# Kernel optimization log

Measured on AMD Instinct MI355X. Metric: run time of the kernel, lower is better.

## Reference

```python
import jax, jax.numpy as jnp
import numpy as np

N = 100000      # nodes
E = 3200000     # edges (avg degree 32)
NFEAT = 512
HID = 64
NCLASS = 64
ALPHA = 0.1
NITER = 10


def setup_inputs() -> dict:
    key = jax.random.key(0)
    k1, k2, k3, k4, k5 = jax.random.split(key, 5)
    x = jax.random.normal(k1, (N, NFEAT), dtype=jnp.float32)
    edge_index = jax.random.randint(k2, (2, E), 0, N, dtype=jnp.int32)
    edge_weight = jax.random.uniform(k3, (E,), dtype=jnp.float32)
    W1 = jax.random.normal(k4, (NFEAT, HID), dtype=jnp.float32) * 0.05
    W2 = jax.random.normal(k5, (HID, NCLASS), dtype=jnp.float32) * 0.05
    return {"x": x, "edge_index": edge_index, "edge_weight": edge_weight,
            "W1": W1, "W2": W2}


def reference(x, edge_index, edge_weight, W1, W2):
    # _transform_features (eval mode: dropout = identity, bias=False)
    h = jax.nn.relu(x @ W1)            # [N, HID]
    z0 = h @ W2                        # [N, NCLASS]
    src = edge_index[0]
    dst = edge_index[1]
    z = z0
    # APPNP power iteration: z = adj @ z + alpha * z0
    for _ in range(NITER):
        msg = edge_weight[:, None] * z[src]                          # [E, NCLASS]
        z = jax.ops.segment_sum(msg, dst, num_segments=N) + ALPHA * z0
    return jax.nn.log_softmax(z, axis=-1)
```

## Files before the change

kernel.cpp:

```cpp
#include <hip/hip_runtime.h>

#define NN     100000
#define EE     3200000
#define NF     512
#define HIDN   64
#define NCLS   64
#define ALPHA  0.1f

#define CHUNK  512
#define NB     196

#define SC_BLOCKS 2048

typedef unsigned short ushort_t;
typedef unsigned int   uint_t;

__device__ inline ushort_t f2bf(float f)
{
    uint_t u = __float_as_uint(f);
    u += 0x7FFFu + ((u >> 16) & 1u);
    return (ushort_t)(u >> 16);
}
__device__ inline float bf2f(ushort_t b)
{
    return __uint_as_float(((uint_t)b) << 16);
}

__device__ inline int2 ldnt_e(const int2* p)
{
    unsigned long long v =
        __builtin_nontemporal_load((const unsigned long long*)p);
    int2 r;
    r.x = (int)(v & 0xFFFFFFFFull);
    r.y = (int)(v >> 32);
    return r;
}

template <bool RELU>
__global__ __launch_bounds__(256) void gemm_kernel(
    const float* __restrict__ A, const float* __restrict__ B,
    float* __restrict__ C, int nrows, int K)
{
    const int BK = 16;
    __shared__ float AsT[BK][68];
    __shared__ float Bs [BK][68];

    int tid = threadIdx.x;
    int tx  = tid & 15;
    int ty  = tid >> 4;
    int rowBase = blockIdx.x * 64;

    int arow = tid >> 2;
    int ak   = (tid & 3) * 4;
    int brow = tid >> 4;
    int bcol = (tid & 15) * 4;

    float acc[4][4] = {};

    for (int k0 = 0; k0 < K; k0 += BK) {
        float4 av;
        int gr = rowBase + arow;
        if (gr < nrows) av = *(const float4*)(A + (size_t)gr * K + k0 + ak);
        else            av = make_float4(0.f, 0.f, 0.f, 0.f);
        float4 bv = *(const float4*)(B + (size_t)(k0 + brow) * 64 + bcol);

        __syncthreads();
        AsT[ak + 0][arow] = av.x;
        AsT[ak + 1][arow] = av.y;
        AsT[ak + 2][arow] = av.z;
        AsT[ak + 3][arow] = av.w;
        *(float4*)&Bs[brow][bcol] = bv;
        __syncthreads();

#pragma unroll
        for (int kk = 0; kk < BK; ++kk) {
            float4 a = *(const float4*)&AsT[kk][ty * 4];
            float4 b = *(const float4*)&Bs [kk][tx * 4];
            acc[0][0] = fmaf(a.x, b.x, acc[0][0]);
            acc[0][1] = fmaf(a.x, b.y, acc[0][1]);
            acc[0][2] = fmaf(a.x, b.z, acc[0][2]);
            acc[0][3] = fmaf(a.x, b.w, acc[0][3]);
            acc[1][0] = fmaf(a.y, b.x, acc[1][0]);
            acc[1][1] = fmaf(a.y, b.y, acc[1][1]);
            acc[1][2] = fmaf(a.y, b.z, acc[1][2]);
            acc[1][3] = fmaf(a.y, b.w, acc[1][3]);
            acc[2][0] = fmaf(a.z, b.x, acc[2][0]);
            acc[2][1] = fmaf(a.z, b.y, acc[2][1]);
            acc[2][2] = fmaf(a.z, b.z, acc[2][2]);
            acc[2][3] = fmaf(a.z, b.w, acc[2][3]);
            acc[3][0] = fmaf(a.w, b.x, acc[3][0]);
            acc[3][1] = fmaf(a.w, b.y, acc[3][1]);
            acc[3][2] = fmaf(a.w, b.z, acc[3][2]);
            acc[3][3] = fmaf(a.w, b.w, acc[3][3]);
        }
    }

#pragma unroll
    for (int i = 0; i < 4; ++i) {
        int r = rowBase + ty * 4 + i;
        if (r < nrows) {
            float4 o;
            o.x = acc[i][0]; o.y = acc[i][1]; o.z = acc[i][2]; o.w = acc[i][3];
            if (RELU) {
                o.x = fmaxf(o.x, 0.f); o.y = fmaxf(o.y, 0.f);
                o.z = fmaxf(o.z, 0.f); o.w = fmaxf(o.w, 0.f);
            }
            *(float4*)(C + (size_t)r * 64 + tx * 4) = o;
        }
    }
}

__global__ __launch_bounds__(256) void gemm2_kernel(
    const float* __restrict__ A, const float* __restrict__ B,
    ushort_t* __restrict__ zb, ushort_t* __restrict__ az, int nrows, int K)
{
    const int BK = 16;
    __shared__ float AsT[BK][68];
    __shared__ float Bs [BK][68];

    int tid = threadIdx.x;
    int tx  = tid & 15;
    int ty  = tid >> 4;
    int rowBase = blockIdx.x * 64;

    int arow = tid >> 2;
    int ak   = (tid & 3) * 4;
    int brow = tid >> 4;
    int bcol = (tid & 15) * 4;

    float acc[4][4] = {};

    for (int k0 = 0; k0 < K; k0 += BK) {
        float4 av;
        int gr = rowBase + arow;
        if (gr < nrows) av = *(const float4*)(A + (size_t)gr * K + k0 + ak);
        else            av = make_float4(0.f, 0.f, 0.f, 0.f);
        float4 bv = *(const float4*)(B + (size_t)(k0 + brow) * 64 + bcol);

        __syncthreads();
        AsT[ak + 0][arow] = av.x;
        AsT[ak + 1][arow] = av.y;
        AsT[ak + 2][arow] = av.z;
        AsT[ak + 3][arow] = av.w;
        *(float4*)&Bs[brow][bcol] = bv;
        __syncthreads();

#pragma unroll
        for (int kk = 0; kk < BK; ++kk) {
            float4 a = *(const float4*)&AsT[kk][ty * 4];
            float4 b = *(const float4*)&Bs [kk][tx * 4];
            acc[0][0] = fmaf(a.x, b.x, acc[0][0]);
            acc[0][1] = fmaf(a.x, b.y, acc[0][1]);
            acc[0][2] = fmaf(a.x, b.z, acc[0][2]);
            acc[0][3] = fmaf(a.x, b.w, acc[0][3]);
            acc[1][0] = fmaf(a.y, b.x, acc[1][0]);
            acc[1][1] = fmaf(a.y, b.y, acc[1][1]);
            acc[1][2] = fmaf(a.y, b.z, acc[1][2]);
            acc[1][3] = fmaf(a.y, b.w, acc[1][3]);
            acc[2][0] = fmaf(a.z, b.x, acc[2][0]);
            acc[2][1] = fmaf(a.z, b.y, acc[2][1]);
            acc[2][2] = fmaf(a.z, b.z, acc[2][2]);
            acc[2][3] = fmaf(a.z, b.w, acc[2][3]);
            acc[3][0] = fmaf(a.w, b.x, acc[3][0]);
            acc[3][1] = fmaf(a.w, b.y, acc[3][1]);
            acc[3][2] = fmaf(a.w, b.z, acc[3][2]);
            acc[3][3] = fmaf(a.w, b.w, acc[3][3]);
        }
    }

#pragma unroll
    for (int i = 0; i < 4; ++i) {
        int r = rowBase + ty * 4 + i;
        if (r < nrows) {
            ushort4 o, oa;
            o.x  = f2bf(acc[i][0]);         o.y  = f2bf(acc[i][1]);
            o.z  = f2bf(acc[i][2]);         o.w  = f2bf(acc[i][3]);
            oa.x = f2bf(ALPHA * acc[i][0]); oa.y = f2bf(ALPHA * acc[i][1]);
            oa.z = f2bf(ALPHA * acc[i][2]); oa.w = f2bf(ALPHA * acc[i][3]);
            *(ushort4*)(zb + (size_t)r * 64 + tx * 4) = o;
            *(ushort4*)(az + (size_t)r * 64 + tx * 4) = oa;
        }
    }
}

__global__ __launch_bounds__(256) void zero_kernel(int* __restrict__ p, int n)
{
    int i = blockIdx.x * 256 + threadIdx.x;
    if (i < n) p[i] = 0;
}

__global__ __launch_bounds__(256) void count_kernel(const int* __restrict__ dst,
                                                    int* __restrict__ deg)
{
    int e = blockIdx.x * 256 + threadIdx.x;
    if (e < EE) atomicAdd(&deg[dst[e]], 1);
}

__global__ __launch_bounds__(256) void scanA_kernel(const int* __restrict__ deg,
                                                    int* __restrict__ bsum)
{
    int b = blockIdx.x, t = threadIdx.x;
    int i = b * CHUNK + t * 2;
    int v = 0;
    if (i < NN)     v += deg[i];
    if (i + 1 < NN) v += deg[i + 1];
    __shared__ int sm[256];
    sm[t] = v;
    __syncthreads();
    for (int o = 128; o > 0; o >>= 1) {
        if (t < o) sm[t] += sm[t + o];
        __syncthreads();
    }
    if (t == 0) bsum[b] = sm[0];
}

__global__ __launch_bounds__(256) void scanB_kernel(const int* __restrict__ bsum,
                                                    int* __restrict__ bbase,
                                                    int* __restrict__ offs)
{
    int t = threadIdx.x;
    int v = (t < NB) ? bsum[t] : 0;
    __shared__ int sm[256];
    sm[t] = v;
    __syncthreads();
    for (int o = 1; o < 256; o <<= 1) {
        int u = (t >= o) ? sm[t - o] : 0;
        __syncthreads();
        sm[t] += u;
        __syncthreads();
    }
    if (t < NB) bbase[t] = sm[t] - v;
    if (t == 0) offs[NN] = EE;
}

__global__ __launch_bounds__(256) void scanC_kernel(const int* __restrict__ deg,
                                                    const int* __restrict__ bbase,
                                                    int* __restrict__ offs,
                                                    int* __restrict__ cursor)
{
    int b = blockIdx.x, t = threadIdx.x;
    int i0 = b * CHUNK + t * 2;
    int d0 = (i0 < NN)     ? deg[i0]     : 0;
    int d1 = (i0 + 1 < NN) ? deg[i0 + 1] : 0;
    int local = d0 + d1;
    __shared__ int sm[256];
    sm[t] = local;
    __syncthreads();
    for (int o = 1; o < 256; o <<= 1) {
        int u = (t >= o) ? sm[t - o] : 0;
        __syncthreads();
        sm[t] += u;
        __syncthreads();
    }
    int excl = sm[t] - local + bbase[b];
    if (i0 < NN)     { offs[i0]     = excl;      cursor[i0]     = excl;      }
    if (i0 + 1 < NN) { offs[i0 + 1] = excl + d0; cursor[i0 + 1] = excl + d0; }
}

__global__ __launch_bounds__(256) void scatter_kernel(
    const int* __restrict__ src, const int* __restrict__ dst,
    const float* __restrict__ w, int* cursor, int2* __restrict__ csr)
{
    const int x      = blockIdx.x & 7;
    const int lo     = x * (NN / 8);
    const int hi     = lo + (NN / 8);
    const int nsl    = gridDim.x >> 3;
    const int stride = nsl * 256;
    for (int e = (blockIdx.x >> 3) * 256 + threadIdx.x; e < EE; e += stride) {
        int d = dst[e];
        if (d >= lo && d < hi) {
            int pos = atomicAdd(&cursor[d], 1);
            csr[pos] = make_int2(src[e], __float_as_int(w[e]));
        }
    }
}

template <bool LSM>
__global__ __launch_bounds__(256) void propagate_kernel(
    const ushort_t* __restrict__ zin, const ushort_t* __restrict__ az0,
    ushort_t* __restrict__ zout_b, float* __restrict__ zout_f,
    const int* __restrict__ offs, const int2* __restrict__ csr)
{
    int gid  = blockIdx.x * 256 + threadIdx.x;
    int node = gid >> 6;
    int lane = gid & 63;
    if (node >= NN) return;

    int beg = offs[node];
    int end = offs[node + 1];
    float acc = 0.f;
    int j = beg;
    for (; j + 8 <= end; j += 8) {
        int2 e0 = ldnt_e(csr + j);     int2 e1 = ldnt_e(csr + j + 1);
        int2 e2 = ldnt_e(csr + j + 2); int2 e3 = ldnt_e(csr + j + 3);
        int2 e4 = ldnt_e(csr + j + 4); int2 e5 = ldnt_e(csr + j + 5);
        int2 e6 = ldnt_e(csr + j + 6); int2 e7 = ldnt_e(csr + j + 7);
        float v0 = bf2f(zin[(size_t)e0.x * 64 + lane]);
        float v1 = bf2f(zin[(size_t)e1.x * 64 + lane]);
        float v2 = bf2f(zin[(size_t)e2.x * 64 + lane]);
        float v3 = bf2f(zin[(size_t)e3.x * 64 + lane]);
        float v4 = bf2f(zin[(size_t)e4.x * 64 + lane]);
        float v5 = bf2f(zin[(size_t)e5.x * 64 + lane]);
        float v6 = bf2f(zin[(size_t)e6.x * 64 + lane]);
        float v7 = bf2f(zin[(size_t)e7.x * 64 + lane]);
        acc = fmaf(__int_as_float(e0.y), v0, acc);
        acc = fmaf(__int_as_float(e1.y), v1, acc);
        acc = fmaf(__int_as_float(e2.y), v2, acc);
        acc = fmaf(__int_as_float(e3.y), v3, acc);
        acc = fmaf(__int_as_float(e4.y), v4, acc);
        acc = fmaf(__int_as_float(e5.y), v5, acc);
        acc = fmaf(__int_as_float(e6.y), v6, acc);
        acc = fmaf(__int_as_float(e7.y), v7, acc);
    }
    for (; j < end; ++j) {
        int2 e = ldnt_e(csr + j);
        acc = fmaf(__int_as_float(e.y), bf2f(zin[(size_t)e.x * 64 + lane]), acc);
    }

    float out = acc + bf2f(az0[(size_t)node * 64 + lane]);

    if (LSM) {
        float m = out;
#pragma unroll
        for (int o = 32; o > 0; o >>= 1) m = fmaxf(m, __shfl_xor(m, o, 64));
        float e = __expf(out - m);
        float s = e;
#pragma unroll
        for (int o = 32; o > 0; o >>= 1) s += __shfl_xor(s, o, 64);
        __builtin_nontemporal_store((out - m) - __logf(s),
                                    zout_f + (size_t)node * 64 + lane);
    } else {
        __builtin_nontemporal_store(f2bf(out),
                                    zout_b + (size_t)node * 64 + lane);
    }
}

extern "C" void kernel_launch(void* const* d_in, const int* in_sizes, int n_in,
                              void* d_out, int out_size, void* d_ws, size_t ws_size,
                              hipStream_t stream)
{
    const float* x  = (const float*)d_in[0];
    const int*   ei = (const int*)  d_in[1];
    const float* ew = (const float*)d_in[2];
    const float* W1 = (const float*)d_in[3];
    const float* W2 = (const float*)d_in[4];
    const int* src = ei;
    const int* dst = ei + EE;

    char* ws = (char*)d_ws;
    size_t off = 0;
    auto alloc = [&](size_t bytes) -> char* {
        char* p = ws + off;
        off += (bytes + 255) & ~(size_t)255;
        return p;
    };

    float*    h     = (float*)   alloc((size_t)NN * HIDN * 4);
    ushort_t* zbA   = (ushort_t*)alloc((size_t)NN * NCLS * 2);
    ushort_t* zbB   = (ushort_t*)alloc((size_t)NN * NCLS * 2);
    ushort_t* az0   = (ushort_t*)alloc((size_t)NN * NCLS * 2);
    int*      deg   = (int*)     alloc((size_t)NN * 4);
    int*      offs  = (int*)     alloc((size_t)(NN + 1) * 4);
    int*      cur_  = (int*)     alloc((size_t)NN * 4);
    int*      bsum  = (int*)     alloc((size_t)NB * 4);
    int*      bbase = (int*)     alloc((size_t)NB * 4);

    int2* csr = (int2*)h;

    gemm_kernel<true><<<(NN + 63) / 64, 256, 0, stream>>>(x, W1, h, NN, NF);
    gemm2_kernel<<<(NN + 63) / 64, 256, 0, stream>>>(h, W2, zbA, az0, NN, HIDN);

    zero_kernel<<<(NN + 255) / 256, 256, 0, stream>>>(deg, NN);
    count_kernel<<<EE / 256, 256, 0, stream>>>(dst, deg);
    scanA_kernel<<<NB, 256, 0, stream>>>(deg, bsum);
    scanB_kernel<<<1, 256, 0, stream>>>(bsum, bbase, offs);
    scanC_kernel<<<NB, 256, 0, stream>>>(deg, bbase, offs, cur_);
    scatter_kernel<<<SC_BLOCKS, 256, 0, stream>>>(src, dst, ew, cur_, csr);

    const ushort_t* cur = zbA;
    ushort_t* nxt = zbB;
    for (int it = 0; it < 9; ++it) {
        propagate_kernel<false><<<(NN * 64) / 256, 256, 0, stream>>>(
            cur, az0, nxt, nullptr, offs, csr);
        ushort_t* t = (ushort_t*)cur; cur = nxt; nxt = t;
    }
    propagate_kernel<true><<<(NN * 64) / 256, 256, 0, stream>>>(
        cur, az0, nullptr, (float*)d_out, offs, csr);
}
```

Measured before the change: 1.885 ms.

## Split node features into 16-class column slabs assigned per XCD for L2 locality

Stores z and alpha*z0 as four column chunks of 16 classes each, and maps blocks so that each pair of XCDs handles one chunk. The gather working set per XCD then shrinks to about 3.2MB and can stay in that XCD's L2. Each wave processes one node with four edge slots in parallel and reduces them with shuffles. Log-softmax moves to a separate kernel because a node's classes are now spread across different blocks. This adds an extra f32 buffer and an extra launch, and each gathered row read is only 32 bytes.

```diff
diff --git a/kernel.cpp b/kernel.cpp
--- a/kernel.cpp
+++ b/kernel.cpp
@@ -7,6 +7,9 @@
 #define NCLS   64
 #define ALPHA  0.1f
 
+#define NC     4
+#define CW     16
+
 #define CHUNK  512
 #define NB     196
 
@@ -34,6 +37,10 @@
     r.x = (int)(v & 0xFFFFFFFFull);
     r.y = (int)(v >> 32);
     return r;
+}
+__device__ inline ushort_t ldnt_u16(const ushort_t* p)
+{
+    return __builtin_nontemporal_load(p);
 }
 
 template <bool RELU>
@@ -168,6 +175,8 @@
         }
     }
 
+    int c = tx >> 2;
+    int k = (tx & 3) * 4;
 #pragma unroll
     for (int i = 0; i < 4; ++i) {
         int r = rowBase + ty * 4 + i;
@@ -177,8 +186,9 @@
             o.z  = f2bf(acc[i][2]);         o.w  = f2bf(acc[i][3]);
             oa.x = f2bf(ALPHA * acc[i][0]); oa.y = f2bf(ALPHA * acc[i][1]);
             oa.z = f2bf(ALPHA * acc[i][2]); oa.w = f2bf(ALPHA * acc[i][3]);
-            *(ushort4*)(zb + (size_t)r * 64 + tx * 4) = o;
-            *(ushort4*)(az + (size_t)r * 64 + tx * 4) = oa;
+            size_t o16 = (size_t)c * (NN * CW) + (size_t)r * CW + k;
+            *(ushort4*)(zb + o16) = o;
+            *(ushort4*)(az + o16) = oa;
         }
     }
 }
@@ -275,64 +285,80 @@
     }
 }
 
-template <bool LSM>
+template <bool FINAL>
 __global__ __launch_bounds__(256) void propagate_kernel(
-    const ushort_t* __restrict__ zin, const ushort_t* __restrict__ az0,
-    ushort_t* __restrict__ zout_b, float* __restrict__ zout_f,
+    const ushort_t* __restrict__ zin,
+    const ushort_t* __restrict__ az0,
+    ushort_t* __restrict__ zout,
+    float* __restrict__ zf,
     const int* __restrict__ offs, const int2* __restrict__ csr)
 {
-    int gid  = blockIdx.x * 256 + threadIdx.x;
-    int node = gid >> 6;
-    int lane = gid & 63;
-    if (node >= NN) return;
+    int bid   = blockIdx.x;
+    int xcd   = bid & 7;
+    int c     = xcd >> 1;
+    int half  = xcd & 1;
+    int g     = bid >> 3;
+    int wave  = threadIdx.x >> 6;
+    int lane  = threadIdx.x & 63;
+    int node  = ((g * 2 + half) << 2) + wave;
+    int cls   = lane & 15;
+    int eslot = lane >> 4;
+
+    const ushort_t* zt = zin + (size_t)c * (NN * CW);
 
     int beg = offs[node];
     int end = offs[node + 1];
     float acc = 0.f;
     int j = beg;
     for (; j + 8 <= end; j += 8) {
-        int2 e0 = ldnt_e(csr + j);     int2 e1 = ldnt_e(csr + j + 1);
-        int2 e2 = ldnt_e(csr + j + 2); int2 e3 = ldnt_e(csr + j + 3);
-        int2 e4 = ldnt_e(csr + j + 4); int2 e5 = ldnt_e(csr + j + 5);
-        int2 e6 = ldnt_e(csr + j + 6); int2 e7 = ldnt_e(csr + j + 7);
-        float v0 = bf2f(zin[(size_t)e0.x * 64 + lane]);
-        float v1 = bf2f(zin[(size_t)e1.x * 64 + lane]);
-        float v2 = bf2f(zin[(size_t)e2.x * 64 + lane]);
-        float v3 = bf2f(zin[(size_t)e3.x * 64 + lane]);
-        float v4 = bf2f(zin[(size_t)e4.x * 64 + lane]);
-        float v5 = bf2f(zin[(size_t)e5.x * 64 + lane]);
-        float v6 = bf2f(zin[(size_t)e6.x * 64 + lane]);
-        float v7 = bf2f(zin[(size_t)e7.x * 64 + lane]);
+        int2 e0 = ldnt_e(csr + j + eslot);
+        int2 e1 = ldnt_e(csr + j + 4 + eslot);
+        float v0 = bf2f(zt[(size_t)e0.x * CW + cls]);
+        float v1 = bf2f(zt[(size_t)e1.x * CW + cls]);
         acc = fmaf(__int_as_float(e0.y), v0, acc);
         acc = fmaf(__int_as_float(e1.y), v1, acc);
-        acc = fmaf(__int_as_float(e2.y), v2, acc);
-        acc = fmaf(__int_as_float(e3.y), v3, acc);
-        acc = fmaf(__int_as_float(e4.y), v4, acc);
-        acc = fmaf(__int_as_float(e5.y), v5, acc);
-        acc = fmaf(__int_as_float(e6.y), v6, acc);
-        acc = fmaf(__int_as_float(e7.y), v7, acc);
-    }
-    for (; j < end; ++j) {
-        int2 e = ldnt_e(csr + j);
-        acc = fmaf(__int_as_float(e.y), bf2f(zin[(size_t)e.x * 64 + lane]), acc);
-    }
-
-    float out = acc + bf2f(az0[(size_t)node * 64 + lane]);
-
-    if (LSM) {
-        float m = out;
-#pragma unroll
-        for (int o = 32; o > 0; o >>= 1) m = fmaxf(m, __shfl_xor(m, o, 64));
-        float e = __expf(out - m);
-        float s = e;
-#pragma unroll
-        for (int o = 32; o > 0; o >>= 1) s += __shfl_xor(s, o, 64);
-        __builtin_nontemporal_store((out - m) - __logf(s),
-                                    zout_f + (size_t)node * 64 + lane);
-    } else {
-        __builtin_nontemporal_store(f2bf(out),
-                                    zout_b + (size_t)node * 64 + lane);
-    }
+    }
+    if (j + 4 <= end) {
+        int2 e = ldnt_e(csr + j + eslot);
+        acc = fmaf(__int_as_float(e.y), bf2f(zt[(size_t)e.x * CW + cls]), acc);
+        j += 4;
+    }
+    int r = end - j;
+    if (eslot < r) {
+        int2 e = ldnt_e(csr + j + eslot);
+        acc = fmaf(__int_as_float(e.y), bf2f(zt[(size_t)e.x * CW + cls]), acc);
+    }
+    acc += __shfl_xor(acc, 16, 64);
+    acc += __shfl_xor(acc, 32, 64);
+
+    size_t o16 = (size_t)c * (NN * CW) + (size_t)node * CW + cls;
+    float out = acc + bf2f(ldnt_u16(az0 + o16));
+    if (eslot == 0) {
+        if (FINAL) zf[o16] = out;
+        else       __builtin_nontemporal_store(f2bf(out), zout + o16);
+    }
+}
+
+template <typename T>
+__global__ __launch_bounds__(256) void lsm_kernel(
+    const T* __restrict__ zf, float* __restrict__ out)
+{
+    int gid  = blockIdx.x * 256 + threadIdx.x;
+    int node = gid >> 6;
+    int lane = gid & 63;
+    if (node >= NN) return;
+    size_t o16 = (size_t)(lane >> 4) * (NN * CW) + (size_t)node * CW + (lane & 15);
+    float v;
+    if (sizeof(T) == 2) v = bf2f(*(const ushort_t*)(zf + o16));
+    else                v = *(const float*)(zf + o16);
+    float m = v;
+#pragma unroll
+    for (int o = 32; o > 0; o >>= 1) m = fmaxf(m, __shfl_xor(m, o, 64));
+    float e = __expf(v - m);
+    float s = e;
+#pragma unroll
+    for (int o = 32; o > 0; o >>= 1) s += __shfl_xor(s, o, 64);
+    out[(size_t)node * 64 + lane] = (v - m) - __logf(s);
 }
 
 extern "C" void kernel_launch(void* const* d_in, const int* in_sizes, int n_in,
@@ -364,6 +390,10 @@
     int*      cur_  = (int*)     alloc((size_t)NN * 4);
     int*      bsum  = (int*)     alloc((size_t)NB * 4);
     int*      bbase = (int*)     alloc((size_t)NB * 4);
+    size_t base_need = off;
+    float*    zf    = (float*)   alloc((size_t)NN * NCLS * 4);
+    bool use_f32 = (off <= ws_size);
+    (void)base_need;
 
     int2* csr = (int2*)h;
 
@@ -377,13 +407,22 @@
     scanC_kernel<<<NB, 256, 0, stream>>>(deg, bbase, offs, cur_);
     scatter_kernel<<<SC_BLOCKS, 256, 0, stream>>>(src, dst, ew, cur_, csr);
 
+    const int PG = NC * (NN / 4);
     const ushort_t* cur = zbA;
     ushort_t* nxt = zbB;
     for (int it = 0; it < 9; ++it) {
-        propagate_kernel<false><<<(NN * 64) / 256, 256, 0, stream>>>(
+        propagate_kernel<false><<<PG, 256, 0, stream>>>(
             cur, az0, nxt, nullptr, offs, csr);
         ushort_t* t = (ushort_t*)cur; cur = nxt; nxt = t;
     }
-    propagate_kernel<true><<<(NN * 64) / 256, 256, 0, stream>>>(
-        cur, az0, nullptr, (float*)d_out, offs, csr);
-}
+    if (use_f32) {
+        propagate_kernel<true><<<PG, 256, 0, stream>>>(
+            cur, az0, nullptr, zf, offs, csr);
+        lsm_kernel<float><<<(NN * 64) / 256, 256, 0, stream>>>(zf, (float*)d_out);
+    } else {
+        propagate_kernel<false><<<PG, 256, 0, stream>>>(
+            cur, az0, nxt, nullptr, offs, csr);
+        lsm_kernel<ushort_t><<<(NN * 64) / 256, 256, 0, stream>>>(
+            nxt, (float*)d_out);
+    }
+}
```

Result: slower. 3.536 ms (+87.6%).
